# Optimization experiments

Hardware: AMD Instinct MI355X
Metric: run time of the kernel (lower is better)

## Reference

```python
import jax, jax.numpy as jnp
import numpy as np

N_HEADS = 32
N_KV_HEADS = 8


def _rope(x, cos, sin):
    # x: [B, S, H, D]; cos/sin: [S, D//2]; complex multiply on consecutive pairs
    B, S, H, D = x.shape
    xr = x.reshape(B, S, H, D // 2, 2)
    x0, x1 = xr[..., 0], xr[..., 1]
    c = cos[None, :, None, :]
    s = sin[None, :, None, :]
    o0 = x0 * c - x1 * s
    o1 = x0 * s + x1 * c
    return jnp.stack([o0, o1], axis=-1).reshape(B, S, H, D)


def setup_inputs():
    key = jax.random.key(0)
    ks = jax.random.split(key, 5)
    B, S, D = 1, 2048, 2048
    hd = D // N_HEADS  # 64
    x = jax.random.normal(ks[0], (B, S, D), jnp.float32)
    wq = jax.random.normal(ks[1], (D, D), jnp.float32) * 0.02
    wk = jax.random.normal(ks[2], (D, N_KV_HEADS * hd), jnp.float32) * 0.02
    wv = jax.random.normal(ks[3], (D, N_KV_HEADS * hd), jnp.float32) * 0.02
    wo = jax.random.normal(ks[4], (D, D), jnp.float32) * 0.02
    # true rotary frequencies (theta_cis = exp(i * pos * freq)), shape [S, hd//2]
    pos = jnp.arange(S, dtype=jnp.float32)
    freqs = 1.0 / (10000.0 ** (jnp.arange(0, hd, 2, dtype=jnp.float32) / hd))
    ang = pos[:, None] * freqs[None, :]
    return {"x": x, "theta_cos": jnp.cos(ang), "theta_sin": jnp.sin(ang),
            "wq": wq, "wk": wk, "wv": wv, "wo": wo}


def reference(x, theta_cos, theta_sin, wq, wk, wv, wo):
    B, S, D = x.shape
    hd = D // N_HEADS
    rep = N_HEADS // N_KV_HEADS
    xq = (x @ wq).reshape(B, S, N_HEADS, hd)
    # NOTE: module applies RoPE to K and V (not Q) - reproduced faithfully
    xk = _rope((x @ wk).reshape(B, S, N_KV_HEADS, hd), theta_cos, theta_sin)
    xv = _rope((x @ wv).reshape(B, S, N_KV_HEADS, hd), theta_cos, theta_sin)
    # GQA: repeat_interleave kv heads along head dim
    xk = jnp.repeat(xk, rep, axis=2)
    xv = jnp.repeat(xv, rep, axis=2)
    att = jnp.einsum('bqhd,bkhd->bhqk', xq, xk) * (hd ** -0.5)
    # faithful to torch.tril + masked_fill(att == 0.0, -inf)
    att = jnp.tril(att)
    att = jnp.where(att == 0.0, -jnp.inf, att)
    att = jax.nn.softmax(att, axis=-1)
    y = jnp.einsum('bhqk,bkhd->bqhd', att, xv).reshape(B, S, D)
    return y @ wo
```

## Files before the change

### kernel.cpp

```cpp
#include <hip/hip_runtime.h>

typedef unsigned short u16;
typedef unsigned int   u32;
typedef __bf16 bf16x8 __attribute__((ext_vector_type(8)));
typedef float  f32x4  __attribute__((ext_vector_type(4)));

__device__ __forceinline__ u16 f2bf(float f) {
    u32 x = __builtin_bit_cast(u32, f);
    x += 0x7fffu + ((x >> 16) & 1u);
    return (u16)(x >> 16);
}
__device__ __forceinline__ float bflo(u32 u) { return __builtin_bit_cast(float, u << 16); }
__device__ __forceinline__ float bfhi(u32 u) { return __builtin_bit_cast(float, u & 0xffff0000u); }

__device__ __forceinline__ bf16x8 ld_frag(const u16* p) {
    return __builtin_bit_cast(bf16x8, *(const uint4*)p);
}

__device__ __forceinline__ f32x4 mfma16(bf16x8 a, bf16x8 b, f32x4 c) {
    return __builtin_amdgcn_mfma_f32_16x16x32_bf16(a, b, c, 0, 0, 0);
}

__device__ __forceinline__ void gl_lds16(const u16* g, u16* l) {
#if __has_builtin(__builtin_amdgcn_global_load_lds)
    __builtin_amdgcn_global_load_lds(
        (__attribute__((address_space(1))) const void*)g,
        (__attribute__((address_space(3))) void*)l, 16, 0, 0);
#else
    *(uint4*)l = *(const uint4*)g;
#endif
}

__device__ __forceinline__ void tr_f2b(const float* __restrict__ in, u16* __restrict__ out,
                                       int R, int C, int c0, int r0, float (*t)[33], int tid) {
    int tx = tid & 31, ty = tid >> 5;
    for (int i = ty; i < 32; i += 8)
        t[i][tx] = in[(size_t)(r0 + i) * C + c0 + tx];
    __syncthreads();
    for (int i = ty; i < 32; i += 8)
        out[(size_t)(c0 + i) * R + r0 + tx] = f2bf(t[tx][i]);
}

__global__ __launch_bounds__(256) void prep(const float* __restrict__ x,
                                            const float* __restrict__ wq,
                                            const float* __restrict__ wk,
                                            const float* __restrict__ wv,
                                            u16* xb, u16* wqT, u16* wkT, u16* wvT) {
    __shared__ float t[32][33];
    int bx = blockIdx.x, tid = threadIdx.x;
    if (bx < 4096) {
        int i = bx * 256 + tid;
        float4 v = ((const float4*)x)[i];
        u32 a = (u32)f2bf(v.x) | ((u32)f2bf(v.y) << 16);
        u32 b = (u32)f2bf(v.z) | ((u32)f2bf(v.w) << 16);
        ((uint2*)xb)[i] = make_uint2(a, b);
    } else if (bx < 8192) {
        int b = bx - 4096;
        tr_f2b(wq, wqT, 2048, 2048, (b & 63) * 32, (b >> 6) * 32, t, tid);
    } else if (bx < 9216) {
        int b = bx - 8192;
        tr_f2b(wk, wkT, 2048, 512, (b & 15) * 32, (b >> 4) * 32, t, tid);
    } else {
        int b = bx - 9216;
        tr_f2b(wv, wvT, 2048, 512, (b & 15) * 32, (b >> 4) * 32, t, tid);
    }
}

__device__ __forceinline__ void gemm_core(const u16* __restrict__ A, const u16* __restrict__ BT,
                                          u16* Cb, int m0, int n0, int N, int Kstride,
                                          int ks, int ke) {
    __shared__ __align__(16) u16 As[128 * 32];
    __shared__ __align__(16) u16 Bs[128 * 32];
    const int tid = threadIdx.x, wave = tid >> 6, lane = tid & 63;
    const int quad = lane >> 4, l15 = lane & 15;
    const int wr = wave >> 1, wc = wave & 1;
    f32x4 acc[4][4] = {};
    for (int k0 = ks; k0 < ke; k0 += 32) {
        const u16* Ag = A + (size_t)m0 * Kstride + k0;
        const u16* Bg = BT + (size_t)n0 * Kstride + k0;
#pragma unroll
        for (int r2 = 0; r2 < 2; r2++) {
            int i = r2 * 256 + tid;
            gl_lds16(Ag + (size_t)(i >> 2) * Kstride + (i & 3) * 8, &As[i * 8]);
            gl_lds16(Bg + (size_t)(i >> 2) * Kstride + (i & 3) * 8, &Bs[i * 8]);
        }
        __syncthreads();
        bf16x8 af[4], bfr[4];
#pragma unroll
        for (int i = 0; i < 4; i++) {
            af[i]  = ld_frag(&As[(wr * 64 + i * 16 + l15) * 32 + quad * 8]);
            bfr[i] = ld_frag(&Bs[(wc * 64 + i * 16 + l15) * 32 + quad * 8]);
        }
#pragma unroll
        for (int i = 0; i < 4; i++)
#pragma unroll
            for (int j = 0; j < 4; j++)
                acc[i][j] = mfma16(af[i], bfr[j], acc[i][j]);
        __syncthreads();
    }
#pragma unroll
    for (int i = 0; i < 4; i++)
#pragma unroll
        for (int r = 0; r < 4; r++) {
            u16* p = Cb + (size_t)(m0 + wr * 64 + i * 16 + quad * 4 + r) * N + n0 + wc * 64 + l15;
#pragma unroll
            for (int j = 0; j < 4; j++) p[j * 16] = f2bf(acc[i][j][r]);
        }
}

__global__ __launch_bounds__(256) void gemm_proj(const u16* __restrict__ A,
                                                 const u16* __restrict__ wqT,
                                                 const u16* __restrict__ wkT,
                                                 const u16* __restrict__ wvT,
                                                 u16* Qp, u16* Kp, u16* Vp) {
    int bx = blockIdx.x, m0 = blockIdx.y * 128, z = blockIdx.z;
    int ks = z * 1024, ke = ks + 1024;
    if (bx < 16)      gemm_core(A, wqT, Qp + (size_t)z * 4194304, m0, bx * 128, 2048, 2048, ks, ke);
    else if (bx < 20) gemm_core(A, wkT, Kp + (size_t)z * 1048576, m0, (bx - 16) * 128, 512, 2048, ks, ke);
    else              gemm_core(A, wvT, Vp + (size_t)z * 1048576, m0, (bx - 20) * 128, 512, 2048, ks, ke);
}

__global__ __launch_bounds__(256) void rope_combine(const u16* __restrict__ Qp,
                                                    const u16* __restrict__ Kp,
                                                    const u16* __restrict__ Vp,
                                                    const float* __restrict__ tc,
                                                    const float* __restrict__ tsn,
                                                    const float* __restrict__ wo,
                                                    u16* Qb, u16* Kb, u16* Vb, u16* woT) {
    __shared__ float t[32][33];
    int bx = blockIdx.x, tid = threadIdx.x;
    if (bx < 4096) {
        int i = bx * 256 + tid;
        uint2 a = ((const uint2*)Qp)[i];
        uint2 b = ((const uint2*)(Qp + 4194304))[i];
        u32 r0_ = (u32)f2bf(bflo(a.x) + bflo(b.x)) | ((u32)f2bf(bfhi(a.x) + bfhi(b.x)) << 16);
        u32 r1_ = (u32)f2bf(bflo(a.y) + bflo(b.y)) | ((u32)f2bf(bfhi(a.y) + bfhi(b.y)) << 16);
        ((uint2*)Qb)[i] = make_uint2(r0_, r1_);
    } else if (bx < 6144) {
        int s = bx - 4096, pr = tid, tt = pr & 31;
        float c = tc[s * 32 + tt], sn = tsn[s * 32 + tt];
        u32 a = ((const u32*)Kp)[s * 256 + pr];
        u32 b = ((const u32*)(Kp + 1048576))[s * 256 + pr];
        float e = bflo(a) + bflo(b), o = bfhi(a) + bfhi(b);
        ((u32*)Kb)[s * 256 + pr] = (u32)f2bf(e * c - o * sn) | ((u32)f2bf(e * sn + o * c) << 16);
    } else if (bx < 8192) {
        int s = bx - 6144, pr = tid, tt = pr & 31;
        float c = tc[s * 32 + tt], sn = tsn[s * 32 + tt];
        u32 a = ((const u32*)Vp)[s * 256 + pr];
        u32 b = ((const u32*)(Vp + 1048576))[s * 256 + pr];
        float e = bflo(a) + bflo(b), o = bfhi(a) + bfhi(b);
        ((u32*)Vb)[s * 256 + pr] = (u32)f2bf(e * c - o * sn) | ((u32)f2bf(e * sn + o * c) << 16);
    } else {
        int b = bx - 8192;
        tr_f2b(wo, woT, 2048, 2048, (b & 63) * 32, (b >> 6) * 32, t, tid);
    }
}

__global__ __launch_bounds__(256) void transpose_b2b(const u16* __restrict__ in,
                                                     u16* __restrict__ out) {
    __shared__ u16 t[32][33];
    int tid = threadIdx.x, tx = tid & 31, ty = tid >> 5;
    int c0 = blockIdx.x * 32, r0 = blockIdx.y * 32;
    for (int i = ty; i < 32; i += 8)
        t[i][tx] = in[(size_t)(r0 + i) * 512 + c0 + tx];
    __syncthreads();
    for (int i = ty; i < 32; i += 8)
        out[(size_t)(c0 + i) * 2048 + r0 + tx] = t[tx][i];
}

#define LPK 72
#define LPV 136
#define T_(q,l,h) (((u32)(q) << 16) | ((u32)(l) << 8) | (u32)(h))
__device__ const u32 ATASK[48] = {
    T_(14,0,15), T_(15,0,16), T_(28,0,16), T_(29,0,16), T_(30,0,16), T_(31,0,16), T_(30,16,31), T_(31,16,32),
    T_(12,0,13), T_(13,0,14), T_(24,0,14), T_(25,0,14), T_(26,0,14), T_(27,0,14), T_(26,14,27), T_(27,14,28),
    T_(28,16,29), T_(29,16,30),
    T_(10,0,11), T_(11,0,12), T_(20,0,12), T_(21,0,12), T_(22,0,12), T_(23,0,12), T_(22,12,23), T_(23,12,24),
    T_(24,14,25), T_(25,14,26),
    T_(8,0,9), T_(9,0,10), T_(16,0,10), T_(17,0,10), T_(18,0,10), T_(19,0,10), T_(18,10,19), T_(19,10,20),
    T_(20,12,21), T_(21,12,22),
    T_(6,0,7), T_(7,0,8), T_(16,10,17), T_(17,10,18),
    T_(4,0,5), T_(5,0,6), T_(2,0,3), T_(3,0,4), T_(0,0,1), T_(1,0,2)
};

struct AttnSmem {
    u16 Ks[128 * LPK];
    u16 Vs[64 * LPV];
    u16 QPs[4 * 16 * LPV];
};

__global__ __launch_bounds__(256) void attn_kernel(const u16* __restrict__ Qb,
                                                   const u16* __restrict__ Kb,
                                                   const u16* __restrict__ VbT,
                                                   u16* __restrict__ Yb,
                                                   float* __restrict__ Opart,
                                                   float* __restrict__ lpart) {
    __shared__ __align__(16) AttnSmem sm;
    const int tid = threadIdx.x, w = tid >> 6, lane = tid & 63;
    const int quad = lane >> 4, l15 = lane & 15;
    const int h = blockIdx.x, kvh = h >> 2;
    const u32 tk = ATASK[blockIdx.y];
    const int qt = tk >> 16, lo = (tk >> 8) & 255, hi = tk & 255;
    const bool partial = (qt >= 16);
    const int pt = partial ? ((qt - 16) * 2 + (lo != 0)) : 0;
    const int q0 = qt * 64;

    const u16* Qg = Qb + (size_t)q0 * 2048 + h * 64;
#pragma unroll
    for (int r2 = 0; r2 < 2; r2++) {
        int i = r2 * 256 + tid, row = i >> 3, c8 = (i & 7) * 8;
        *(uint4*)&sm.QPs[row * LPK + c8] = *(const uint4*)(Qg + (size_t)row * 2048 + c8);
    }
    __syncthreads();
    bf16x8 aQ0 = ld_frag(&sm.QPs[(w * 16 + l15) * LPK + quad * 8]);
    bf16x8 aQ1 = ld_frag(&sm.QPs[(w * 16 + l15) * LPK + 32 + quad * 8]);

    f32x4 O[4] = {};
    float l_acc[4] = {0.f, 0.f, 0.f, 0.f};
    u16* Ps = &sm.QPs[w * 16 * LPV];
    const int qrow = q0 + w * 16 + quad * 4;

    for (int jt = lo; jt < hi; jt += 2) {
        const int j0 = jt * 64;
        __syncthreads();
        const u16* Kg = Kb + (size_t)j0 * 512 + kvh * 64;
        const u16* Vg = VbT + (size_t)(kvh * 64) * 2048 + j0;
#pragma unroll
        for (int r2 = 0; r2 < 4; r2++) {
            int i = r2 * 256 + tid;
            int krow = i >> 3, kc = (i & 7) * 8;
            *(uint4*)&sm.Ks[krow * LPK + kc] = *(const uint4*)(Kg + (size_t)krow * 512 + kc);
            int vrow = i >> 4, vc = (i & 15) * 8;
            *(uint4*)&sm.Vs[vrow * LPV + vc] = *(const uint4*)(Vg + (size_t)vrow * 2048 + vc);
        }
        __syncthreads();

        f32x4 s[8];
#pragma unroll
        for (int j = 0; j < 8; j++) {
            bf16x8 b0 = ld_frag(&sm.Ks[(j * 16 + l15) * LPK + quad * 8]);
            bf16x8 b1 = ld_frag(&sm.Ks[(j * 16 + l15) * LPK + 32 + quad * 8]);
            f32x4 z = {};
            z = mfma16(aQ0, b0, z);
            z = mfma16(aQ1, b1, z);
            s[j] = z;
        }
        if (jt + 1 >= qt) {
#pragma unroll
            for (int j = 0; j < 8; j++)
#pragma unroll
                for (int r = 0; r < 4; r++) {
                    float p = __expf(s[j][r] * 0.125f);
                    if ((j0 + j * 16 + l15) > (qrow + r)) p = 0.f;
                    s[j][r] = p; l_acc[r] += p;
                }
        } else {
#pragma unroll
            for (int j = 0; j < 8; j++)
#pragma unroll
                for (int r = 0; r < 4; r++) {
                    float p = __expf(s[j][r] * 0.125f);
                    s[j][r] = p; l_acc[r] += p;
                }
        }
#pragma unroll
        for (int j = 0; j < 8; j++)
#pragma unroll
            for (int r = 0; r < 4; r++)
                Ps[(quad * 4 + r) * LPV + j * 16 + l15] = f2bf(s[j][r]);
        bf16x8 aP[4];
#pragma unroll
        for (int kk = 0; kk < 4; kk++)
            aP[kk] = ld_frag(&Ps[l15 * LPV + kk * 32 + quad * 8]);
#pragma unroll
        for (int j = 0; j < 4; j++)
#pragma unroll
            for (int kk = 0; kk < 4; kk++) {
                bf16x8 v = ld_frag(&sm.Vs[(j * 16 + l15) * LPV + kk * 32 + quad * 8]);
                O[j] = mfma16(aP[kk], v, O[j]);
            }
    }
    float l_i[4];
#pragma unroll
    for (int r = 0; r < 4; r++) {
        float rs = l_acc[r];
        rs += __shfl_xor(rs, 1); rs += __shfl_xor(rs, 2);
        rs += __shfl_xor(rs, 4); rs += __shfl_xor(rs, 8);
        l_i[r] = rs;
    }
    if (!partial) {
#pragma unroll
        for (int r = 0; r < 4; r++) {
            float inv = __frcp_rn(l_i[r]);
#pragma unroll
            for (int j = 0; j < 4; j++)
                Yb[(size_t)(q0 + w * 16 + quad * 4 + r) * 2048 + h * 64 + j * 16 + l15] =
                    f2bf(O[j][r] * inv);
        }
    } else {
        float* Og = Opart + ((size_t)(pt * 32 + h) * 64) * 64;
#pragma unroll
        for (int r = 0; r < 4; r++) {
            int row = w * 16 + quad * 4 + r;
#pragma unroll
            for (int j = 0; j < 4; j++)
                Og[(size_t)row * 64 + j * 16 + l15] = O[j][r];
            if (l15 == 0) lpart[(size_t)(pt * 32 + h) * 64 + row] = l_i[r];
        }
    }
}

__global__ void combine_kernel(const float* __restrict__ Opart,
                               const float* __restrict__ lpart,
                               u16* __restrict__ Yb) {
    int e = blockIdx.x * 256 + threadIdx.x;
    int d4 = e & 15, h = (e >> 4) & 31, rg = e >> 9;
    int t16 = rg >> 6, row = rg & 63;
    int s0 = (t16 * 2) * 32 + h, s1 = s0 + 32;
    float4 a = ((const float4*)Opart)[((size_t)s0 * 64 + row) * 16 + d4];
    float4 b = ((const float4*)Opart)[((size_t)s1 * 64 + row) * 16 + d4];
    float l = lpart[(size_t)s0 * 64 + row] + lpart[(size_t)s1 * 64 + row];
    float inv = __frcp_rn(l);
    u32 lo = (u32)f2bf((a.x + b.x) * inv) | ((u32)f2bf((a.y + b.y) * inv) << 16);
    u32 hi = (u32)f2bf((a.z + b.z) * inv) | ((u32)f2bf((a.w + b.w) * inv) << 16);
    int q = 1024 + rg;
    ((uint2*)(Yb + (size_t)q * 2048 + h * 64))[d4] = make_uint2(lo, hi);
}

__global__ __launch_bounds__(256) void gemm_out_split(const u16* __restrict__ A,
                                                      const u16* __restrict__ BT,
                                                      u16* C0, u16* C1, u16* C2, u16* C3) {
    int z = blockIdx.z;
    u16* dst = z == 0 ? C0 : z == 1 ? C1 : z == 2 ? C2 : C3;
    gemm_core(A, BT, dst, blockIdx.y * 128, blockIdx.x * 128, 2048, 2048, z * 512, (z + 1) * 512);
}

__global__ void combine_out(const u16* __restrict__ C0, const u16* __restrict__ C1,
                            const u16* __restrict__ C2, const u16* __restrict__ C3,
                            float* __restrict__ out) {
    int i = blockIdx.x * 256 + threadIdx.x;
    uint2 a = ((const uint2*)C0)[i], b = ((const uint2*)C1)[i];
    uint2 c = ((const uint2*)C2)[i], d = ((const uint2*)C3)[i];
    float4 o;
    o.x = bflo(a.x) + bflo(b.x) + bflo(c.x) + bflo(d.x);
    o.y = bfhi(a.x) + bfhi(b.x) + bfhi(c.x) + bfhi(d.x);
    o.z = bflo(a.y) + bflo(b.y) + bflo(c.y) + bflo(d.y);
    o.w = bfhi(a.y) + bfhi(b.y) + bfhi(c.y) + bfhi(d.y);
    ((float4*)out)[i] = o;
}

extern "C" void kernel_launch(void* const* d_in, const int* in_sizes, int n_in,
                              void* d_out, int out_size, void* d_ws, size_t ws_size,
                              hipStream_t stream) {
    const float* x  = (const float*)d_in[0];
    const float* tc = (const float*)d_in[1];
    const float* ts = (const float*)d_in[2];
    const float* wq = (const float*)d_in[3];
    const float* wk = (const float*)d_in[4];
    const float* wv = (const float*)d_in[5];
    const float* wo = (const float*)d_in[6];
    float* out = (float*)d_out;

    char* w = (char*)d_ws;
    u16*   xb   = (u16*)(w);
    u16*   wqT  = (u16*)(w + (8u  << 20));
    u16*   wkT  = (u16*)(w + (16u << 20));
    u16*   wvT  = (u16*)(w + (18u << 20));
    u16*   Qp   = (u16*)(w + (20u << 20));
    u16*   Kp   = (u16*)(w + (36u << 20));
    u16*   Vp   = (u16*)(w + (40u << 20));
    u16*   Qb   = (u16*)(w);
    u16*   woT  = (u16*)(w + (8u  << 20));
    u16*   Kb   = (u16*)(w + (16u << 20));
    u16*   Vb   = (u16*)(w + (18u << 20));
    u16*   VbT  = (u16*)(w + (20u << 20));
    float* lpart= (float*)(w + (22u << 20));
    u16*   Yb   = (u16*)(w + (24u << 20));
    float* Opart= (float*)(w + (32u << 20));
    u16*   C0   = (u16*)(w);
    u16*   C1   = (u16*)(w + (16u << 20));
    u16*   C2   = (u16*)(w + (32u << 20));
    u16*   C3   = (u16*)(w + (40u << 20));

    prep<<<10240, 256, 0, stream>>>(x, wq, wk, wv, xb, wqT, wkT, wvT);
    gemm_proj<<<dim3(24, 16, 2), 256, 0, stream>>>(xb, wqT, wkT, wvT, Qp, Kp, Vp);
    rope_combine<<<12288, 256, 0, stream>>>(Qp, Kp, Vp, tc, ts, wo, Qb, Kb, Vb, woT);
    transpose_b2b<<<dim3(16, 64), 256, 0, stream>>>(Vb, VbT);
    attn_kernel<<<dim3(32, 48), 256, 0, stream>>>(Qb, Kb, VbT, Yb, Opart, lpart);
    combine_kernel<<<2048, 256, 0, stream>>>(Opart, lpart, Yb);
    gemm_out_split<<<dim3(16, 16, 4), 256, 0, stream>>>(Yb, woT, C0, C1, C2, C3);
    combine_out<<<4096, 256, 0, stream>>>(C0, C1, C2, C3, out);
}
```

Measured before the change: 260.3 us.

## Process all four GQA query heads per block to share K/V tiles

The attention kernel now assigns one block per KV head instead of per query head. It loads each 64-row K/V tile into shared memory once and reuses it across the four query heads that share it, with per-head P buffers and accumulators held in registers. This cuts redundant global K/V loads fourfold and shrinks the tile step from 128 to 64 keys. The trade-off is a 4x smaller grid (384 blocks) and higher register pressure, which may hurt occupancy and load balance across CUs.

Result: faster. 250.9 us (-3.6%).

```diff
diff --git a/kernel.cpp b/kernel.cpp
--- a/kernel.cpp
+++ b/kernel.cpp
@@ -169,7 +169,7 @@
 }
 
 #define LPK 72
-#define LPV 136
+#define PSTR 1152
 #define T_(q,l,h) (((u32)(q) << 16) | ((u32)(l) << 8) | (u32)(h))
 __device__ const u32 ATASK[48] = {
     T_(14,0,15), T_(15,0,16), T_(28,0,16), T_(29,0,16), T_(30,0,16), T_(31,0,16), T_(30,16,31), T_(31,16,32),
@@ -184,128 +184,142 @@
 };
 
 struct AttnSmem {
-    u16 Ks[128 * LPK];
-    u16 Vs[64 * LPV];
-    u16 QPs[4 * 16 * LPV];
+    u16 Ks[64 * LPK];
+    u16 Vs[64 * LPK];
+    u16 Ps[16 * PSTR];
 };
 
-__global__ __launch_bounds__(256) void attn_kernel(const u16* __restrict__ Qb,
-                                                   const u16* __restrict__ Kb,
-                                                   const u16* __restrict__ VbT,
-                                                   u16* __restrict__ Yb,
-                                                   float* __restrict__ Opart,
-                                                   float* __restrict__ lpart) {
+__global__ __launch_bounds__(256, 2) void attn_kernel(const u16* __restrict__ Qb,
+                                                      const u16* __restrict__ Kb,
+                                                      const u16* __restrict__ VbT,
+                                                      u16* __restrict__ Yb,
+                                                      float* __restrict__ Opart,
+                                                      float* __restrict__ lpart) {
     __shared__ __align__(16) AttnSmem sm;
     const int tid = threadIdx.x, w = tid >> 6, lane = tid & 63;
     const int quad = lane >> 4, l15 = lane & 15;
-    const int h = blockIdx.x, kvh = h >> 2;
+    const int kvh = blockIdx.x, h_base = kvh * 4;
     const u32 tk = ATASK[blockIdx.y];
     const int qt = tk >> 16, lo = (tk >> 8) & 255, hi = tk & 255;
     const bool partial = (qt >= 16);
     const int pt = partial ? ((qt - 16) * 2 + (lo != 0)) : 0;
     const int q0 = qt * 64;
-
-    const u16* Qg = Qb + (size_t)q0 * 2048 + h * 64;
-#pragma unroll
-    for (int r2 = 0; r2 < 2; r2++) {
-        int i = r2 * 256 + tid, row = i >> 3, c8 = (i & 7) * 8;
-        *(uint4*)&sm.QPs[row * LPK + c8] = *(const uint4*)(Qg + (size_t)row * 2048 + c8);
-    }
-    __syncthreads();
-    bf16x8 aQ0 = ld_frag(&sm.QPs[(w * 16 + l15) * LPK + quad * 8]);
-    bf16x8 aQ1 = ld_frag(&sm.QPs[(w * 16 + l15) * LPK + 32 + quad * 8]);
-
-    f32x4 O[4] = {};
-    float l_acc[4] = {0.f, 0.f, 0.f, 0.f};
-    u16* Ps = &sm.QPs[w * 16 * LPV];
     const int qrow = q0 + w * 16 + quad * 4;
 
-    for (int jt = lo; jt < hi; jt += 2) {
+    bf16x8 aQ[4][2];
+    const u16* qp = Qb + (size_t)(q0 + w * 16 + l15) * 2048 + h_base * 64 + quad * 8;
+#pragma unroll
+    for (int hh = 0; hh < 4; hh++) {
+        aQ[hh][0] = __builtin_bit_cast(bf16x8, *(const uint4*)(qp + hh * 64));
+        aQ[hh][1] = __builtin_bit_cast(bf16x8, *(const uint4*)(qp + hh * 64 + 32));
+    }
+
+    f32x4 O[4][4] = {};
+    float l_acc[4][4] = {};
+
+    for (int jt = lo; jt < hi; jt++) {
         const int j0 = jt * 64;
         __syncthreads();
         const u16* Kg = Kb + (size_t)j0 * 512 + kvh * 64;
         const u16* Vg = VbT + (size_t)(kvh * 64) * 2048 + j0;
 #pragma unroll
-        for (int r2 = 0; r2 < 4; r2++) {
+        for (int r2 = 0; r2 < 2; r2++) {
             int i = r2 * 256 + tid;
-            int krow = i >> 3, kc = (i & 7) * 8;
-            *(uint4*)&sm.Ks[krow * LPK + kc] = *(const uint4*)(Kg + (size_t)krow * 512 + kc);
-            int vrow = i >> 4, vc = (i & 15) * 8;
-            *(uint4*)&sm.Vs[vrow * LPV + vc] = *(const uint4*)(Vg + (size_t)vrow * 2048 + vc);
+            *(uint4*)&sm.Ks[(i >> 3) * LPK + (i & 7) * 8] = *(const uint4*)(Kg + (size_t)(i >> 3) * 512 + (i & 7) * 8);
+            *(uint4*)&sm.Vs[(i >> 3) * LPK + (i & 7) * 8] = *(const uint4*)(Vg + (size_t)(i >> 3) * 2048 + (i & 7) * 8);
         }
         __syncthreads();
 
-        f32x4 s[8];
-#pragma unroll
-        for (int j = 0; j < 8; j++) {
-            bf16x8 b0 = ld_frag(&sm.Ks[(j * 16 + l15) * LPK + quad * 8]);
-            bf16x8 b1 = ld_frag(&sm.Ks[(j * 16 + l15) * LPK + 32 + quad * 8]);
-            f32x4 z = {};
-            z = mfma16(aQ0, b0, z);
-            z = mfma16(aQ1, b1, z);
-            s[j] = z;
-        }
-        if (jt + 1 >= qt) {
-#pragma unroll
-            for (int j = 0; j < 8; j++)
-#pragma unroll
-                for (int r = 0; r < 4; r++) {
-                    float p = __expf(s[j][r] * 0.125f);
-                    if ((j0 + j * 16 + l15) > (qrow + r)) p = 0.f;
-                    s[j][r] = p; l_acc[r] += p;
-                }
+        bf16x8 bK[4][2];
+#pragma unroll
+        for (int j = 0; j < 4; j++) {
+            bK[j][0] = ld_frag(&sm.Ks[(j * 16 + l15) * LPK + quad * 8]);
+            bK[j][1] = ld_frag(&sm.Ks[(j * 16 + l15) * LPK + 32 + quad * 8]);
+        }
+        const bool diag = (jt == qt);
+#pragma unroll
+        for (int hh = 0; hh < 4; hh++) {
+            f32x4 s[4];
+#pragma unroll
+            for (int j = 0; j < 4; j++) {
+                f32x4 z = {};
+                z = mfma16(aQ[hh][0], bK[j][0], z);
+                z = mfma16(aQ[hh][1], bK[j][1], z);
+                s[j] = z;
+            }
+            u16* Ph = &sm.Ps[(hh * 4 + w) * PSTR];
+            if (diag) {
+#pragma unroll
+                for (int j = 0; j < 4; j++)
+#pragma unroll
+                    for (int r = 0; r < 4; r++) {
+                        float p = __expf(s[j][r] * 0.125f);
+                        if ((j0 + j * 16 + l15) > (qrow + r)) p = 0.f;
+                        s[j][r] = p; l_acc[hh][r] += p;
+                    }
+            } else {
+#pragma unroll
+                for (int j = 0; j < 4; j++)
+#pragma unroll
+                    for (int r = 0; r < 4; r++) {
+                        float p = __expf(s[j][r] * 0.125f);
+                        s[j][r] = p; l_acc[hh][r] += p;
+                    }
+            }
+#pragma unroll
+            for (int j = 0; j < 4; j++)
+#pragma unroll
+                for (int r = 0; r < 4; r++)
+                    Ph[(quad * 4 + r) * LPK + j * 16 + l15] = f2bf(s[j][r]);
+        }
+        bf16x8 bV[4][2];
+#pragma unroll
+        for (int j = 0; j < 4; j++) {
+            bV[j][0] = ld_frag(&sm.Vs[(j * 16 + l15) * LPK + quad * 8]);
+            bV[j][1] = ld_frag(&sm.Vs[(j * 16 + l15) * LPK + 32 + quad * 8]);
+        }
+#pragma unroll
+        for (int hh = 0; hh < 4; hh++) {
+            const u16* Ph = &sm.Ps[(hh * 4 + w) * PSTR];
+            bf16x8 aP0 = ld_frag(&Ph[l15 * LPK + quad * 8]);
+            bf16x8 aP1 = ld_frag(&Ph[l15 * LPK + 32 + quad * 8]);
+#pragma unroll
+            for (int j = 0; j < 4; j++) {
+                O[hh][j] = mfma16(aP0, bV[j][0], O[hh][j]);
+                O[hh][j] = mfma16(aP1, bV[j][1], O[hh][j]);
+            }
+        }
+    }
+#pragma unroll
+    for (int hh = 0; hh < 4; hh++) {
+        const int h = h_base + hh;
+        float l_i[4];
+#pragma unroll
+        for (int r = 0; r < 4; r++) {
+            float rs = l_acc[hh][r];
+            rs += __shfl_xor(rs, 1); rs += __shfl_xor(rs, 2);
+            rs += __shfl_xor(rs, 4); rs += __shfl_xor(rs, 8);
+            l_i[r] = rs;
+        }
+        if (!partial) {
+#pragma unroll
+            for (int r = 0; r < 4; r++) {
+                float inv = __frcp_rn(l_i[r]);
+#pragma unroll
+                for (int j = 0; j < 4; j++)
+                    Yb[(size_t)(q0 + w * 16 + quad * 4 + r) * 2048 + h * 64 + j * 16 + l15] =
+                        f2bf(O[hh][j][r] * inv);
+            }
         } else {
-#pragma unroll
-            for (int j = 0; j < 8; j++)
-#pragma unroll
-                for (int r = 0; r < 4; r++) {
-                    float p = __expf(s[j][r] * 0.125f);
-                    s[j][r] = p; l_acc[r] += p;
-                }
-        }
-#pragma unroll
-        for (int j = 0; j < 8; j++)
-#pragma unroll
-            for (int r = 0; r < 4; r++)
-                Ps[(quad * 4 + r) * LPV + j * 16 + l15] = f2bf(s[j][r]);
-        bf16x8 aP[4];
-#pragma unroll
-        for (int kk = 0; kk < 4; kk++)
-            aP[kk] = ld_frag(&Ps[l15 * LPV + kk * 32 + quad * 8]);
-#pragma unroll
-        for (int j = 0; j < 4; j++)
-#pragma unroll
-            for (int kk = 0; kk < 4; kk++) {
-                bf16x8 v = ld_frag(&sm.Vs[(j * 16 + l15) * LPV + kk * 32 + quad * 8]);
-                O[j] = mfma16(aP[kk], v, O[j]);
+            float* Og = Opart + ((size_t)(pt * 32 + h) * 64) * 64;
+#pragma unroll
+            for (int r = 0; r < 4; r++) {
+                int row = w * 16 + quad * 4 + r;
+#pragma unroll
+                for (int j = 0; j < 4; j++)
+                    Og[(size_t)row * 64 + j * 16 + l15] = O[hh][j][r];
+                if (l15 == 0) lpart[(size_t)(pt * 32 + h) * 64 + row] = l_i[r];
             }
-    }
-    float l_i[4];
-#pragma unroll
-    for (int r = 0; r < 4; r++) {
-        float rs = l_acc[r];
-        rs += __shfl_xor(rs, 1); rs += __shfl_xor(rs, 2);
-        rs += __shfl_xor(rs, 4); rs += __shfl_xor(rs, 8);
-        l_i[r] = rs;
-    }
-    if (!partial) {
-#pragma unroll
-        for (int r = 0; r < 4; r++) {
-            float inv = __frcp_rn(l_i[r]);
-#pragma unroll
-            for (int j = 0; j < 4; j++)
-                Yb[(size_t)(q0 + w * 16 + quad * 4 + r) * 2048 + h * 64 + j * 16 + l15] =
-                    f2bf(O[j][r] * inv);
-        }
-    } else {
-        float* Og = Opart + ((size_t)(pt * 32 + h) * 64) * 64;
-#pragma unroll
-        for (int r = 0; r < 4; r++) {
-            int row = w * 16 + quad * 4 + r;
-#pragma unroll
-            for (int j = 0; j < 4; j++)
-                Og[(size_t)row * 64 + j * 16 + l15] = O[j][r];
-            if (l15 == 0) lpart[(size_t)(pt * 32 + h) * 64 + row] = l_i[r];
         }
     }
 }
@@ -386,7 +400,7 @@
     gemm_proj<<<dim3(24, 16, 2), 256, 0, stream>>>(xb, wqT, wkT, wvT, Qp, Kp, Vp);
     rope_combine<<<12288, 256, 0, stream>>>(Qp, Kp, Vp, tc, ts, wo, Qb, Kb, Vb, woT);
     transpose_b2b<<<dim3(16, 64), 256, 0, stream>>>(Vb, VbT);
-    attn_kernel<<<dim3(32, 48), 256, 0, stream>>>(Qb, Kb, VbT, Yb, Opart, lpart);
+    attn_kernel<<<dim3(8, 48), 256, 0, stream>>>(Qb, Kb, VbT, Yb, Opart, lpart);
     combine_kernel<<<2048, 256, 0, stream>>>(Opart, lpart, Yb);
     gemm_out_split<<<dim3(16, 16, 4), 256, 0, stream>>>(Yb, woT, C0, C1, C2, C3);
     combine_out<<<4096, 256, 0, stream>>>(C0, C1, C2, C3, out);
```
